# Kernel tuning notes

Hardware: AMD Instinct MI355X
Metric: run time of the kernel (lower is better)

The kernel has to match this reference:

```python
import jax, jax.numpy as jnp
import numpy as np
import math

C = 256
N_HEAD = 8
GROUPS = 16
EPS = 1e-5


def group_norm(x, w, b):
    # x: [B, C, H, W]; biased variance over (group_channels, H, W), like torch GroupNorm
    B, Cc, H, W = x.shape
    xg = x.reshape(B, GROUPS, Cc // GROUPS, H, W)
    mean = xg.mean(axis=(2, 3, 4), keepdims=True)
    var = ((xg - mean) ** 2).mean(axis=(2, 3, 4), keepdims=True)
    xn = ((xg - mean) * jax.lax.rsqrt(var + EPS)).reshape(B, Cc, H, W)
    return xn * w[None, :, None, None] + b[None, :, None, None]


def setup_inputs() -> dict:
    key = jax.random.key(0)
    k0, k1, k2, k3, k4, k5 = jax.random.split(key, 6)
    B, H, W = 4, 48, 48
    input_feat = jax.random.normal(k0, (B, C, H, W), dtype=jnp.float32)
    gn_weight = jnp.ones((C,), dtype=jnp.float32) + 0.02 * jax.random.normal(k1, (C,), dtype=jnp.float32)
    gn_bias = 0.02 * jax.random.normal(k2, (C,), dtype=jnp.float32)
    w_qkv = jax.random.normal(k3, (3 * C, C), dtype=jnp.float32) / math.sqrt(C)  # Conv2d 1x1, no bias
    w_out = jax.random.normal(k4, (C, C), dtype=jnp.float32) / math.sqrt(C)      # Conv2d 1x1
    b_out = 0.02 * jax.random.normal(k5, (C,), dtype=jnp.float32)
    return {"input_feat": input_feat, "gn_weight": gn_weight, "gn_bias": gn_bias,
            "w_qkv": w_qkv, "w_out": w_out, "b_out": b_out}


def reference(input_feat, gn_weight, gn_bias, w_qkv, w_out, b_out):
    # H=W=48 <= max_attn_size=48 -> full attention branch
    B, Cc, H, W = input_feat.shape
    n, d = N_HEAD, Cc // N_HEAD
    S = H * W
    normed = group_norm(input_feat, gn_weight, gn_bias)
    # 1x1 conv QKV: [B, 3C, H, W]
    qkv = jnp.einsum('oc,bchw->bohw', w_qkv, normed)
    # view(B, n, 3*d, H, W).chunk(3, dim=2) == reshape to (B, n, 3, d, S)
    qkv = qkv.reshape(B, n, 3, d, S)
    q, k, v = qkv[:, :, 0], qkv[:, :, 1], qkv[:, :, 2]  # each [B, n, d, S]
    # NOTE: original divides by sqrt(channel), not sqrt(head_dim)
    scale = 1.0 / math.sqrt(Cc)
    scores = jnp.einsum('bnds,bndt->bnst', q, k) * scale  # [B, n, S, S]
    attn = jax.nn.softmax(scores, axis=-1)
    o = jnp.einsum('bnst,bndt->bnds', attn, v)  # [B, n, d, S]
    o = o.reshape(B, Cc, H, W)
    out = jnp.einsum('oc,bchw->bohw', w_out, o) + b_out[None, :, None, None]
    return out + input_feat
```

## Files before the change

kernel.cpp:

```cpp
#include <hip/hip_runtime.h>
#include <hip/hip_bf16.h>
#include <stdint.h>

#define S    2304
#define CHN  256
#define BATCH 4
#define NKEYS 1152
#define QS   0.09016844005556021f

typedef __attribute__((ext_vector_type(8))) short bf16x8;
typedef __attribute__((ext_vector_type(4))) float f32x4;
typedef __attribute__((ext_vector_type(2))) uint32_t u32x2;
typedef __attribute__((ext_vector_type(4))) unsigned short u16x4;
typedef unsigned short u16;

#define AS1 __attribute__((address_space(1)))
#define AS3 __attribute__((address_space(3)))
#define GLDS(gptr, lptr) __builtin_amdgcn_global_load_lds((const AS1 void*)(gptr), (AS3 void*)(lptr), 16, 0, 0)

__device__ __forceinline__ u16 f2bf(float f) {
  union { float f; uint32_t u; } v; v.f = f;
  uint32_t u = v.u;
  u += 0x7fffu + ((u >> 16) & 1u);
  return (u16)(u >> 16);
}
__device__ __forceinline__ float bf2f(u16 h) {
  union { uint32_t u; float f; } v; v.u = ((uint32_t)h) << 16;
  return v.f;
}
__device__ __forceinline__ uint32_t pk_bf16(float a, float b) {
  union { __hip_bfloat162 h; uint32_t u; } cv;
  cv.h = __float22bfloat162_rn(make_float2(a, b));
  return cv.u;
}

__global__ void k_prep(const float* __restrict__ wq, const float* __restrict__ wo,
                       u16* __restrict__ wq_bf, u16* __restrict__ wo_bf) {
  int i = blockIdx.x * 256 + threadIdx.x;
  if (i < 768 * 256) wq_bf[i] = f2bf(wq[i]);
  int j = i - 768 * 256;
  if (j >= 0 && j < 256 * 256) wo_bf[j] = f2bf(wo[j]);
}

__global__ void k_gnstats(const float* __restrict__ x, float2* __restrict__ stats) {
  int bg = blockIdx.x;
  const float4* p = (const float4*)(x + (size_t)bg * 36864);
  float s = 0.f, ss = 0.f;
  for (int i = threadIdx.x; i < 9216; i += 1024) {
    float4 v = p[i];
    s  += v.x + v.y + v.z + v.w;
    ss += v.x * v.x + v.y * v.y + v.z * v.z + v.w * v.w;
  }
  int lane = threadIdx.x & 63, wv = threadIdx.x >> 6;
  for (int m = 1; m < 64; m <<= 1) { s += __shfl_xor(s, m, 64); ss += __shfl_xor(ss, m, 64); }
  __shared__ float rs[16], rss[16];
  if (lane == 0) { rs[wv] = s; rss[wv] = ss; }
  __syncthreads();
  if (threadIdx.x == 0) {
    float S_ = 0.f, SS = 0.f;
    for (int i = 0; i < 16; ++i) { S_ += rs[i]; SS += rss[i]; }
    float mean = S_ / 36864.f;
    float var  = SS / 36864.f - mean * mean;
    stats[bg] = make_float2(mean, rsqrtf(var + 1e-5f));
  }
}

__global__ void k_gnnorm(const float* __restrict__ x, const float* __restrict__ w,
                         const float* __restrict__ bias, const float2* __restrict__ stats,
                         u16* __restrict__ nt) {
  int bid = blockIdx.x;
  int b = bid / 144, r = bid % 144;
  int sblk = r >> 2, cq = r & 3;
  int t = threadIdx.x;
  int ni = t & 63, cgrp = t >> 6;
  int s = sblk * 64 + ni;
  int cbase = cq * 64 + cgrp * 16;
  float2 stg = stats[b * 16 + (cbase >> 4)];
  bf16x8 v0, v1;
  #pragma unroll
  for (int e = 0; e < 16; ++e) {
    int c = cbase + e;
    float val = x[(size_t)(b * 256 + c) * S + s];
    float xn = (val - stg.x) * stg.y * w[c] + bias[c];
    if (e < 8) v0[e] = (short)f2bf(xn); else v1[e - 8] = (short)f2bf(xn);
  }
  u16* dst = nt + (size_t)(b * S + s) * 256 + cbase;
  *(bf16x8*)dst = v0;
  *(bf16x8*)(dst + 8) = v1;
}

__global__ __launch_bounds__(256) void k_qkv(const u16* __restrict__ A,
                                             const u16* __restrict__ Bm,
                                             u16* __restrict__ qkt,
                                             u16* __restrict__ vt) {
  __shared__ __align__(16) u16 As[2][64 * 32];
  __shared__ __align__(16) u16 Bs[2][128 * 32];
  int tid = threadIdx.x, lane = tid & 63, w = tid >> 6;
  int wr = w >> 1, wc = w & 1;
  int cb = lane & 15, q4 = lane >> 4;
  int m0 = blockIdx.y * 64, n0 = blockIdx.x * 128;

  const u16* gA0 = A  + (size_t)(m0 + (tid >> 2)) * 256 + (tid & 3) * 8;
  const u16* gB0 = Bm + (size_t)(n0 + (tid >> 2)) * 256 + (tid & 3) * 8;
  const u16* gB1 = gB0 + 64 * 256;
  char* lA = (char*)&As[0][0] + (w << 10);
  char* lB = (char*)&Bs[0][0] + (w << 10);

  #define STAGE_Q(buf, k0) do {                      \
    GLDS(gA0 + (k0), lA + (buf) * 4096);             \
    GLDS(gB0 + (k0), lB + (buf) * 8192);             \
    GLDS(gB1 + (k0), lB + (buf) * 8192 + 4096);      \
  } while (0)

  f32x4 zero4 = {0.f, 0.f, 0.f, 0.f};
  f32x4 acc[2][4];
  for (int i = 0; i < 2; ++i) for (int j = 0; j < 4; ++j) acc[i][j] = zero4;

  STAGE_Q(0, 0);
  __syncthreads();
  for (int ks = 0; ks < 8; ++ks) {
    int cur = ks & 1;
    if (ks < 7) STAGE_Q(cur ^ 1, (ks + 1) * 32);
    const u16* as = &As[cur][0];
    const u16* bs = &Bs[cur][0];
    bf16x8 af[2], bfr[4];
    for (int i = 0; i < 2; ++i)
      af[i]  = *(const bf16x8*)&as[(wr * 32 + i * 16 + cb) * 32 + 8 * q4];
    for (int j = 0; j < 4; ++j)
      bfr[j] = *(const bf16x8*)&bs[(wc * 64 + j * 16 + cb) * 32 + 8 * q4];
    for (int i = 0; i < 2; ++i)
      for (int j = 0; j < 4; ++j)
        acc[i][j] = __builtin_amdgcn_mfma_f32_16x16x32_bf16(af[i], bfr[j], acc[i][j], 0, 0, 0);
    __syncthreads();
  }

  for (int i = 0; i < 2; ++i)
    for (int j = 0; j < 4; ++j) {
      int ob = m0 + wr * 32 + i * 16 + q4 * 4;
      int n  = n0 + wc * 64 + j * 16 + cb;
      int h = ob / 96, oq = ob % 96;
      if (oq < 64) {
        float sc = (oq < 32) ? QS : 1.f;
        u16x4 pk;
        for (int r = 0; r < 4; ++r) pk[r] = f2bf(acc[i][j][r] * sc);
        *(u16x4*)&qkt[(size_t)n * 512 + h * 64 + oq] = pk;
      } else {
        for (int r = 0; r < 4; ++r)
          vt[(size_t)(h * 32 + oq - 64 + r) * 9216 + n] = f2bf(acc[i][j][r]);
      }
    }
  #undef STAGE_Q
}

__global__ __launch_bounds__(256) void k_attn(const u16* __restrict__ qkt,
                                              const u16* __restrict__ vt,
                                              u16* __restrict__ otP,
                                              float* __restrict__ lsum) {
  __shared__ __align__(16) u16 Ks[2][64 * 32];
  __shared__ __align__(16) u16 Vd[2][32 * 64];
  __shared__ __align__(16) u16 Ps[4][16 * 64];

  int tid = threadIdx.x, lane = tid & 63, w = tid >> 6;
  int cb = lane & 15, g4 = lane >> 4;
  int hw = blockIdx.x;
  int orig = (hw & 7) * 288 + (hw >> 3);
  int bh = orig / 72, rem = orig % 72;
  int qtile = rem >> 1, split = rem & 1;
  int b = bh >> 3, h = bh & 7;
  int q0 = qtile * 64 + w * 16;

  const u16* kbase = qkt + (size_t)(b * S) * 512 + h * 64 + 32 + (size_t)split * NKEYS * 512;
  const u16* vbase = vt + (size_t)(h * 32) * 9216 + (size_t)b * S + split * NKEYS;

  bf16x8 qf = *(const bf16x8*)&qkt[(size_t)(b * S + q0 + cb) * 512 + h * 64 + 8 * g4];

  f32x4 zero4 = {0.f, 0.f, 0.f, 0.f};
  f32x4 acc_o[2]; acc_o[0] = zero4; acc_o[1] = zero4;
  float l = 0.f;

  int xk = (cb ^ (cb >> 2)) & 3;
  int sw7 = cb & 7;

  const u16* p_kf[4];
  #pragma unroll
  for (int k4 = 0; k4 < 4; ++k4)
    p_kf[k4] = &Ks[0][(16 * k4 + cb) * 32 + ((g4 ^ xk) * 8)];
  u16* p_pw[4];
  #pragma unroll
  for (int k4 = 0; k4 < 4; ++k4)
    p_pw[k4] = &Ps[w][cb * 64 + (((2 * k4 + (g4 >> 1)) ^ sw7) << 3) + ((g4 & 1) << 2)];
  const u16* p_pa[2];
  #pragma unroll
  for (int kk = 0; kk < 2; ++kk)
    p_pa[kk] = &Ps[w][cb * 64 + (((4 * kk + g4) ^ sw7) << 3)];
  const u16* p_vb[2][2];
  #pragma unroll
  for (int jd = 0; jd < 2; ++jd)
    #pragma unroll
    for (int kk = 0; kk < 2; ++kk)
      p_vb[jd][kk] = &Vd[0][(16 * jd + cb) * 64 + (((4 * kk + g4) ^ sw7) << 3)];

  int krow = tid >> 2, kch = (tid & 3) ^ ((krow ^ (krow >> 2)) & 3);
  int vrow = tid >> 3, vch = (tid & 7) ^ (vrow & 7);
  const u16* gK = kbase + (size_t)krow * 512 + kch * 8;
  const u16* gV = vbase + (size_t)vrow * 9216 + vch * 8;
  char* ldsK = (char*)&Ks[0][0] + (w << 10);
  char* ldsV = (char*)&Vd[0][0] + (w << 10);

  #define STAGE_A(buf) do {                          \
    GLDS(gK, ldsK + (buf) * 4096);                   \
    GLDS(gV, ldsV + (buf) * 4096);                   \
    gK += 64 * 512; gV += 64;                        \
  } while (0)

  #define TILE(buf, pf) do {                                                   \
    if (pf) STAGE_A(buf ^ 1);                                                  \
    bf16x8 kf[4];                                                              \
    _Pragma("unroll")                                                          \
    for (int k4 = 0; k4 < 4; ++k4)                                             \
      kf[k4] = *(const bf16x8*)(p_kf[k4] + (buf) * 2048);                      \
    f32x4 pacc[4];                                                             \
    __builtin_amdgcn_s_setprio(1);                                             \
    _Pragma("unroll")                                                          \
    for (int k4 = 0; k4 < 4; ++k4)                                             \
      pacc[k4] = __builtin_amdgcn_mfma_f32_16x16x32_bf16(kf[k4], qf, zero4, 0, 0, 0); \
    __builtin_amdgcn_s_setprio(0);                                             \
    float lacc = 0.f;                                                          \
    _Pragma("unroll")                                                          \
    for (int k4 = 0; k4 < 4; ++k4) {                                           \
      f32x4 p = pacc[k4];                                                      \
      float e0 = __builtin_amdgcn_exp2f(p[0]);                                 \
      float e1 = __builtin_amdgcn_exp2f(p[1]);                                 \
      float e2 = __builtin_amdgcn_exp2f(p[2]);                                 \
      float e3 = __builtin_amdgcn_exp2f(p[3]);                                 \
      lacc += (e0 + e1) + (e2 + e3);                                           \
      u32x2 pk = { pk_bf16(e0, e1), pk_bf16(e2, e3) };                         \
      *(u32x2*)p_pw[k4] = pk;                                                  \
    }                                                                          \
    l += lacc;                                                                 \
    asm volatile("s_waitcnt lgkmcnt(0)" ::: "memory");                         \
    __builtin_amdgcn_sched_barrier(0);                                         \
    __builtin_amdgcn_s_setprio(1);                                             \
    bf16x8 pa[2];                                                              \
    _Pragma("unroll")                                                          \
    for (int kk = 0; kk < 2; ++kk)                                             \
      pa[kk] = *(const bf16x8*)p_pa[kk];                                       \
    _Pragma("unroll")                                                          \
    for (int jd = 0; jd < 2; ++jd)                                             \
      _Pragma("unroll")                                                        \
      for (int kk = 0; kk < 2; ++kk) {                                         \
        bf16x8 vb = *(const bf16x8*)(p_vb[jd][kk] + (buf) * 2048);             \
        acc_o[jd] = __builtin_amdgcn_mfma_f32_16x16x32_bf16(pa[kk], vb, acc_o[jd], 0, 0, 0); \
      }                                                                        \
    __builtin_amdgcn_s_setprio(0);                                             \
    __syncthreads();                                                           \
  } while (0)

  STAGE_A(0);
  __syncthreads();
  for (int it = 0; it < 9; ++it) {
    TILE(0, 1);
    TILE(1, it < 8);
  }

  float v = l;
  v += __shfl_xor(v, 16, 64);
  v += __shfl_xor(v, 32, 64);
  if (lane < 16)
    lsum[(size_t)(bh * 2 + split) * S + q0 + lane] = v;

  u16* op = otP + (size_t)split * 9216 * 256;
  for (int r = 0; r < 4; ++r) {
    int sq = q0 + 4 * g4 + r;
    for (int jd = 0; jd < 2; ++jd) {
      int c = h * 32 + 16 * jd + cb;
      op[(size_t)(b * S + sq) * 256 + c] = f2bf(acc_o[jd][r]);
    }
  }
  #undef STAGE_A
  #undef TILE
}

__global__ void k_comb(const u16* __restrict__ otP, const float* __restrict__ lsum,
                       u16* __restrict__ ot) {
  int gid = blockIdx.x * 256 + threadIdx.x;
  int n = gid >> 5, c8 = gid & 31;
  int b = n / S, s = n - b * S;
  int h = c8 >> 2;
  float l0 = lsum[(size_t)((b * 8 + h) * 2 + 0) * S + s];
  float l1 = lsum[(size_t)((b * 8 + h) * 2 + 1) * S + s];
  float inv = __builtin_amdgcn_rcpf(l0 + l1);
  bf16x8 a = *(const bf16x8*)&otP[(size_t)n * 256 + c8 * 8];
  bf16x8 bb = *(const bf16x8*)&otP[(size_t)9216 * 256 + (size_t)n * 256 + c8 * 8];
  bf16x8 o;
  #pragma unroll
  for (int e = 0; e < 8; ++e)
    o[e] = (short)f2bf((bf2f((u16)a[e]) + bf2f((u16)bb[e])) * inv);
  *(bf16x8*)&ot[(size_t)n * 256 + c8 * 8] = o;
}

__global__ __launch_bounds__(256) void k_oproj(const u16* __restrict__ A,
                                               const u16* __restrict__ Bm,
                                               float* __restrict__ out,
                                               const float* __restrict__ bias,
                                               const float* __restrict__ resid) {
  __shared__ __align__(16) u16 As[2][64 * 32];
  __shared__ __align__(16) u16 Bs[2][64 * 32];
  int tid = threadIdx.x, lane = tid & 63, w = tid >> 6;
  int cb = lane & 15, q4 = lane >> 4;
  int m0 = blockIdx.y * 64, n0 = blockIdx.x * 64;

  const u16* gA0 = A  + (size_t)(m0 + (tid >> 2)) * 256 + (tid & 3) * 8;
  const u16* gB0 = Bm + (size_t)(n0 + (tid >> 2)) * 256 + (tid & 3) * 8;
  char* lA = (char*)&As[0][0] + (w << 10);
  char* lB = (char*)&Bs[0][0] + (w << 10);

  #define STAGE_O(buf, k0) do {                      \
    GLDS(gA0 + (k0), lA + (buf) * 4096);             \
    GLDS(gB0 + (k0), lB + (buf) * 4096);             \
  } while (0)

  f32x4 zero4 = {0.f, 0.f, 0.f, 0.f};
  f32x4 acc[4];
  for (int j = 0; j < 4; ++j) acc[j] = zero4;

  STAGE_O(0, 0);
  __syncthreads();
  for (int ks = 0; ks < 8; ++ks) {
    int cur = ks & 1;
    if (ks < 7) STAGE_O(cur ^ 1, (ks + 1) * 32);
    const u16* as = &As[cur][0];
    const u16* bs = &Bs[cur][0];
    bf16x8 af = *(const bf16x8*)&as[(w * 16 + cb) * 32 + 8 * q4];
    bf16x8 bfr[4];
    for (int j = 0; j < 4; ++j)
      bfr[j] = *(const bf16x8*)&bs[(j * 16 + cb) * 32 + 8 * q4];
    for (int j = 0; j < 4; ++j)
      acc[j] = __builtin_amdgcn_mfma_f32_16x16x32_bf16(af, bfr[j], acc[j], 0, 0, 0);
    __syncthreads();
  }

  for (int j = 0; j < 4; ++j)
    for (int r = 0; r < 4; ++r) {
      int o = m0 + w * 16 + q4 * 4 + r;
      int n = n0 + j * 16 + cb;
      int b = n / S, s2 = n % S;
      size_t gi = (size_t)(b * 256 + o) * S + s2;
      out[gi] = acc[j][r] + bias[o] + resid[gi];
    }
  #undef STAGE_O
}

extern "C" void kernel_launch(void* const* d_in, const int* in_sizes, int n_in,
                              void* d_out, int out_size, void* d_ws, size_t ws_size,
                              hipStream_t stream) {
  const float* input = (const float*)d_in[0];
  const float* gnw   = (const float*)d_in[1];
  const float* gnb   = (const float*)d_in[2];
  const float* wqkv  = (const float*)d_in[3];
  const float* wout  = (const float*)d_in[4];
  const float* bout  = (const float*)d_in[5];
  float* out = (float*)d_out;
  char* ws = (char*)d_ws;

  size_t o_wq  = 0;
  size_t o_wo  = o_wq + (size_t)768 * 256 * 2;
  size_t o_st  = o_wo + (size_t)256 * 256 * 2;
  size_t o_nt  = o_st + 1024;
  size_t o_qkt = o_nt + (size_t)9216 * 256 * 2;
  size_t o_vt  = o_qkt + (size_t)9216 * 512 * 2;
  size_t o_oP  = o_vt + (size_t)256 * 9216 * 2;
  size_t o_ls  = o_oP + (size_t)2 * 9216 * 256 * 2;

  u16*    wq_bf = (u16*)(ws + o_wq);
  u16*    wo_bf = (u16*)(ws + o_wo);
  float2* stats = (float2*)(ws + o_st);
  u16*    nt    = (u16*)(ws + o_nt);
  u16*    qkt   = (u16*)(ws + o_qkt);
  u16*    vt    = (u16*)(ws + o_vt);
  u16*    otP   = (u16*)(ws + o_oP);
  float*  lsum  = (float*)(ws + o_ls);
  u16*    otb   = (u16*)(ws + o_nt);

  k_prep<<<1024, 256, 0, stream>>>(wqkv, wout, wq_bf, wo_bf);
  k_gnstats<<<64, 1024, 0, stream>>>(input, stats);
  k_gnnorm<<<576, 256, 0, stream>>>(input, gnw, gnb, stats, nt);
  k_qkv<<<dim3(72, 12), 256, 0, stream>>>(wq_bf, nt, qkt, vt);
  k_attn<<<2304, 256, 0, stream>>>(qkt, vt, otP, lsum);
  k_comb<<<1152, 256, 0, stream>>>(otP, lsum, otb);
  k_oproj<<<dim3(144, 4), 256, 0, stream>>>(wo_bf, otb, out, bout, input);
}
```

Before: 93.21 us.

## Merge attention key-split halves in-block, drop combine kernel, split GN stats

The attention kernel now runs both key halves in one 512-thread block, with 8 waves split into two groups of 4. The two partial outputs and row sums are combined through LDS before the normalized bf16 output is written, so the separate combine kernel and its global partial buffers go away. Row sums are now computed with an MFMA against a ones vector instead of scalar adds. GroupNorm stats are split across 4 blocks per group using atomics, and the zeroing is moved into the prep kernel. The larger blocks may lower occupancy, and the float atomics make the summation order nondeterministic.

Result: faster. 88.82 us (-4.7%).

```diff
diff --git a/kernel.cpp b/kernel.cpp
--- a/kernel.cpp
+++ b/kernel.cpp
@@ -35,38 +35,40 @@
 }
 
 __global__ void k_prep(const float* __restrict__ wq, const float* __restrict__ wo,
-                       u16* __restrict__ wq_bf, u16* __restrict__ wo_bf) {
+                       u16* __restrict__ wq_bf, u16* __restrict__ wo_bf,
+                       float* __restrict__ sraw) {
   int i = blockIdx.x * 256 + threadIdx.x;
+  if (blockIdx.x == 0 && threadIdx.x < 128) sraw[threadIdx.x] = 0.f;
   if (i < 768 * 256) wq_bf[i] = f2bf(wq[i]);
   int j = i - 768 * 256;
   if (j >= 0 && j < 256 * 256) wo_bf[j] = f2bf(wo[j]);
 }
 
-__global__ void k_gnstats(const float* __restrict__ x, float2* __restrict__ stats) {
-  int bg = blockIdx.x;
-  const float4* p = (const float4*)(x + (size_t)bg * 36864);
+__global__ void k_gnstats(const float* __restrict__ x, float* __restrict__ sraw) {
+  int blk = blockIdx.x;
+  int bg = blk >> 2, part = blk & 3;
+  const float4* p = (const float4*)(x + (size_t)bg * 36864) + part * 2304;
   float s = 0.f, ss = 0.f;
-  for (int i = threadIdx.x; i < 9216; i += 1024) {
+  for (int i = threadIdx.x; i < 2304; i += 256) {
     float4 v = p[i];
     s  += v.x + v.y + v.z + v.w;
     ss += v.x * v.x + v.y * v.y + v.z * v.z + v.w * v.w;
   }
   int lane = threadIdx.x & 63, wv = threadIdx.x >> 6;
   for (int m = 1; m < 64; m <<= 1) { s += __shfl_xor(s, m, 64); ss += __shfl_xor(ss, m, 64); }
-  __shared__ float rs[16], rss[16];
+  __shared__ float rs[4], rss[4];
   if (lane == 0) { rs[wv] = s; rss[wv] = ss; }
   __syncthreads();
   if (threadIdx.x == 0) {
-    float S_ = 0.f, SS = 0.f;
-    for (int i = 0; i < 16; ++i) { S_ += rs[i]; SS += rss[i]; }
-    float mean = S_ / 36864.f;
-    float var  = SS / 36864.f - mean * mean;
-    stats[bg] = make_float2(mean, rsqrtf(var + 1e-5f));
+    float S_ = rs[0] + rs[1] + rs[2] + rs[3];
+    float SS = rss[0] + rss[1] + rss[2] + rss[3];
+    atomicAdd(&sraw[bg * 2], S_);
+    atomicAdd(&sraw[bg * 2 + 1], SS);
   }
 }
 
 __global__ void k_gnnorm(const float* __restrict__ x, const float* __restrict__ w,
-                         const float* __restrict__ bias, const float2* __restrict__ stats,
+                         const float* __restrict__ bias, const float* __restrict__ sraw,
                          u16* __restrict__ nt) {
   int bid = blockIdx.x;
   int b = bid / 144, r = bid % 144;
@@ -75,13 +77,17 @@
   int ni = t & 63, cgrp = t >> 6;
   int s = sblk * 64 + ni;
   int cbase = cq * 64 + cgrp * 16;
-  float2 stg = stats[b * 16 + (cbase >> 4)];
+  int bgi = b * 16 + (cbase >> 4);
+  float sx = sraw[bgi * 2], ssx = sraw[bgi * 2 + 1];
+  float mean = sx * (1.f / 36864.f);
+  float var  = ssx * (1.f / 36864.f) - mean * mean;
+  float rstd = rsqrtf(var + 1e-5f);
   bf16x8 v0, v1;
   #pragma unroll
   for (int e = 0; e < 16; ++e) {
     int c = cbase + e;
     float val = x[(size_t)(b * 256 + c) * S + s];
-    float xn = (val - stg.x) * stg.y * w[c] + bias[c];
+    float xn = (val - mean) * rstd * w[c] + bias[c];
     if (e < 8) v0[e] = (short)f2bf(xn); else v1[e - 8] = (short)f2bf(xn);
   }
   u16* dst = nt + (size_t)(b * S + s) * 256 + cbase;
@@ -152,31 +158,34 @@
   #undef STAGE_Q
 }
 
-__global__ __launch_bounds__(256) void k_attn(const u16* __restrict__ qkt,
+__global__ __launch_bounds__(512) void k_attn(const u16* __restrict__ qkt,
                                               const u16* __restrict__ vt,
-                                              u16* __restrict__ otP,
-                                              float* __restrict__ lsum) {
-  __shared__ __align__(16) u16 Ks[2][64 * 32];
-  __shared__ __align__(16) u16 Vd[2][32 * 64];
-  __shared__ __align__(16) u16 Ps[4][16 * 64];
+                                              u16* __restrict__ ot) {
+  __shared__ __align__(16) u16 Ks[2][2][2048];
+  __shared__ __align__(16) u16 Vd[2][2][2048];
+  __shared__ __align__(16) u16 Ps[8][1024];
+  __shared__ float Ls[8][16];
 
   int tid = threadIdx.x, lane = tid & 63, w = tid >> 6;
   int cb = lane & 15, g4 = lane >> 4;
+  int qw = w & 3, half = w >> 2;
   int hw = blockIdx.x;
-  int orig = (hw & 7) * 288 + (hw >> 3);
-  int bh = orig / 72, rem = orig % 72;
-  int qtile = rem >> 1, split = rem & 1;
+  int orig = (hw & 7) * 144 + (hw >> 3);
+  int bh = orig / 36, qtile = orig % 36;
   int b = bh >> 3, h = bh & 7;
-  int q0 = qtile * 64 + w * 16;
-
-  const u16* kbase = qkt + (size_t)(b * S) * 512 + h * 64 + 32 + (size_t)split * NKEYS * 512;
-  const u16* vbase = vt + (size_t)(h * 32) * 9216 + (size_t)b * S + split * NKEYS;
+  int q0 = qtile * 64 + qw * 16;
+
+  const u16* kbase = qkt + (size_t)(b * S) * 512 + h * 64 + 32 + (size_t)half * NKEYS * 512;
+  const u16* vbase = vt + (size_t)(h * 32) * 9216 + (size_t)b * S + half * NKEYS;
 
   bf16x8 qf = *(const bf16x8*)&qkt[(size_t)(b * S + q0 + cb) * 512 + h * 64 + 8 * g4];
+  bf16x8 vones;
+  #pragma unroll
+  for (int e = 0; e < 8; ++e) vones[e] = (short)0x3F80;
 
   f32x4 zero4 = {0.f, 0.f, 0.f, 0.f};
   f32x4 acc_o[2]; acc_o[0] = zero4; acc_o[1] = zero4;
-  float l = 0.f;
+  f32x4 lacc4 = zero4;
 
   int xk = (cb ^ (cb >> 2)) & 3;
   int sw7 = cb & 7;
@@ -184,7 +193,7 @@
   const u16* p_kf[4];
   #pragma unroll
   for (int k4 = 0; k4 < 4; ++k4)
-    p_kf[k4] = &Ks[0][(16 * k4 + cb) * 32 + ((g4 ^ xk) * 8)];
+    p_kf[k4] = &Ks[half][0][(16 * k4 + cb) * 32 + ((g4 ^ xk) * 8)];
   u16* p_pw[4];
   #pragma unroll
   for (int k4 = 0; k4 < 4; ++k4)
@@ -198,14 +207,15 @@
   for (int jd = 0; jd < 2; ++jd)
     #pragma unroll
     for (int kk = 0; kk < 2; ++kk)
-      p_vb[jd][kk] = &Vd[0][(16 * jd + cb) * 64 + (((4 * kk + g4) ^ sw7) << 3)];
-
-  int krow = tid >> 2, kch = (tid & 3) ^ ((krow ^ (krow >> 2)) & 3);
-  int vrow = tid >> 3, vch = (tid & 7) ^ (vrow & 7);
+      p_vb[jd][kk] = &Vd[half][0][(16 * jd + cb) * 64 + (((4 * kk + g4) ^ sw7) << 3)];
+
+  int tloc = tid & 255;
+  int krow = tloc >> 2, kch = (tloc & 3) ^ ((krow ^ (krow >> 2)) & 3);
+  int vrow = tloc >> 3, vch = (tloc & 7) ^ (vrow & 7);
   const u16* gK = kbase + (size_t)krow * 512 + kch * 8;
   const u16* gV = vbase + (size_t)vrow * 9216 + vch * 8;
-  char* ldsK = (char*)&Ks[0][0] + (w << 10);
-  char* ldsV = (char*)&Vd[0][0] + (w << 10);
+  char* ldsK = (char*)&Ks[half][0][0] + (qw << 10);
+  char* ldsV = (char*)&Vd[half][0][0] + (qw << 10);
 
   #define STAGE_A(buf) do {                          \
     GLDS(gK, ldsK + (buf) * 4096);                   \
@@ -225,7 +235,6 @@
     for (int k4 = 0; k4 < 4; ++k4)                                             \
       pacc[k4] = __builtin_amdgcn_mfma_f32_16x16x32_bf16(kf[k4], qf, zero4, 0, 0, 0); \
     __builtin_amdgcn_s_setprio(0);                                             \
-    float lacc = 0.f;                                                          \
     _Pragma("unroll")                                                          \
     for (int k4 = 0; k4 < 4; ++k4) {                                           \
       f32x4 p = pacc[k4];                                                      \
@@ -233,11 +242,9 @@
       float e1 = __builtin_amdgcn_exp2f(p[1]);                                 \
       float e2 = __builtin_amdgcn_exp2f(p[2]);                                 \
       float e3 = __builtin_amdgcn_exp2f(p[3]);                                 \
-      lacc += (e0 + e1) + (e2 + e3);                                           \
       u32x2 pk = { pk_bf16(e0, e1), pk_bf16(e2, e3) };                         \
       *(u32x2*)p_pw[k4] = pk;                                                  \
     }                                                                          \
-    l += lacc;                                                                 \
     asm volatile("s_waitcnt lgkmcnt(0)" ::: "memory");                         \
     __builtin_amdgcn_sched_barrier(0);                                         \
     __builtin_amdgcn_s_setprio(1);                                             \
@@ -245,6 +252,8 @@
     _Pragma("unroll")                                                          \
     for (int kk = 0; kk < 2; ++kk)                                             \
       pa[kk] = *(const bf16x8*)p_pa[kk];                                       \
+    lacc4 = __builtin_amdgcn_mfma_f32_16x16x32_bf16(pa[0], vones, lacc4, 0, 0, 0); \
+    lacc4 = __builtin_amdgcn_mfma_f32_16x16x32_bf16(pa[1], vones, lacc4, 0, 0, 0); \
     _Pragma("unroll")                                                          \
     for (int jd = 0; jd < 2; ++jd)                                             \
       _Pragma("unroll")                                                        \
@@ -263,40 +272,29 @@
     TILE(1, it < 8);
   }
 
-  float v = l;
-  v += __shfl_xor(v, 16, 64);
-  v += __shfl_xor(v, 32, 64);
-  if (lane < 16)
-    lsum[(size_t)(bh * 2 + split) * S + q0 + lane] = v;
-
-  u16* op = otP + (size_t)split * 9216 * 256;
+  float* PsF = (float*)&Ps[w][0];
+  #pragma unroll
+  for (int jd = 0; jd < 2; ++jd)
+    *(f32x4*)&PsF[(cb + 16 * jd) * 16 + 4 * g4] = acc_o[jd];
+  if (cb == 0)
+    *(f32x4*)&Ls[w][4 * g4] = lacc4;
+  __syncthreads();
+
+  const float* A0 = (const float*)&Ps[qw][0];
+  const float* A1 = (const float*)&Ps[qw + 4][0];
+  int dd = half * 16 + cb;
+  f32x4 s0 = *(const f32x4*)&A0[dd * 16 + 4 * g4];
+  f32x4 s1 = *(const f32x4*)&A1[dd * 16 + 4 * g4];
+  f32x4 lt0 = *(const f32x4*)&Ls[qw][4 * g4];
+  f32x4 lt1 = *(const f32x4*)&Ls[qw + 4][4 * g4];
+  #pragma unroll
   for (int r = 0; r < 4; ++r) {
+    float inv = __builtin_amdgcn_rcpf(lt0[r] + lt1[r]);
     int sq = q0 + 4 * g4 + r;
-    for (int jd = 0; jd < 2; ++jd) {
-      int c = h * 32 + 16 * jd + cb;
-      op[(size_t)(b * S + sq) * 256 + c] = f2bf(acc_o[jd][r]);
-    }
+    ot[(size_t)(b * S + sq) * 256 + h * 32 + dd] = f2bf((s0[r] + s1[r]) * inv);
   }
   #undef STAGE_A
   #undef TILE
-}
-
-__global__ void k_comb(const u16* __restrict__ otP, const float* __restrict__ lsum,
-                       u16* __restrict__ ot) {
-  int gid = blockIdx.x * 256 + threadIdx.x;
-  int n = gid >> 5, c8 = gid & 31;
-  int b = n / S, s = n - b * S;
-  int h = c8 >> 2;
-  float l0 = lsum[(size_t)((b * 8 + h) * 2 + 0) * S + s];
-  float l1 = lsum[(size_t)((b * 8 + h) * 2 + 1) * S + s];
-  float inv = __builtin_amdgcn_rcpf(l0 + l1);
-  bf16x8 a = *(const bf16x8*)&otP[(size_t)n * 256 + c8 * 8];
-  bf16x8 bb = *(const bf16x8*)&otP[(size_t)9216 * 256 + (size_t)n * 256 + c8 * 8];
-  bf16x8 o;
-  #pragma unroll
-  for (int e = 0; e < 8; ++e)
-    o[e] = (short)f2bf((bf2f((u16)a[e]) + bf2f((u16)bb[e])) * inv);
-  *(bf16x8*)&ot[(size_t)n * 256 + c8 * 8] = o;
 }
 
 __global__ __launch_bounds__(256) void k_oproj(const u16* __restrict__ A,
@@ -369,24 +367,19 @@
   size_t o_nt  = o_st + 1024;
   size_t o_qkt = o_nt + (size_t)9216 * 256 * 2;
   size_t o_vt  = o_qkt + (size_t)9216 * 512 * 2;
-  size_t o_oP  = o_vt + (size_t)256 * 9216 * 2;
-  size_t o_ls  = o_oP + (size_t)2 * 9216 * 256 * 2;
 
   u16*    wq_bf = (u16*)(ws + o_wq);
   u16*    wo_bf = (u16*)(ws + o_wo);
-  float2* stats = (float2*)(ws + o_st);
+  float*  sraw  = (float*)(ws + o_st);
   u16*    nt    = (u16*)(ws + o_nt);
   u16*    qkt   = (u16*)(ws + o_qkt);
   u16*    vt    = (u16*)(ws + o_vt);
-  u16*    otP   = (u16*)(ws + o_oP);
-  float*  lsum  = (float*)(ws + o_ls);
   u16*    otb   = (u16*)(ws + o_nt);
 
-  k_prep<<<1024, 256, 0, stream>>>(wqkv, wout, wq_bf, wo_bf);
-  k_gnstats<<<64, 1024, 0, stream>>>(input, stats);
-  k_gnnorm<<<576, 256, 0, stream>>>(input, gnw, gnb, stats, nt);
+  k_prep<<<1024, 256, 0, stream>>>(wqkv, wout, wq_bf, wo_bf, sraw);
+  k_gnstats<<<256, 256, 0, stream>>>(input, sraw);
+  k_gnnorm<<<576, 256, 0, stream>>>(input, gnw, gnb, sraw, nt);
   k_qkv<<<dim3(72, 12), 256, 0, stream>>>(wq_bf, nt, qkt, vt);
-  k_attn<<<2304, 256, 0, stream>>>(qkt, vt, otP, lsum);
-  k_comb<<<1152, 256, 0, stream>>>(otP, lsum, otb);
+  k_attn<<<1152, 512, 0, stream>>>(qkt, vt, otb);
   k_oproj<<<dim3(144, 4), 256, 0, stream>>>(wo_bf, otb, out, bout, input);
 }
```
